# Kernel optimization log

Measured on AMD Instinct MI355X. Metric: run time of the kernel, lower is better.

The kernel has to match this reference:

```python
import jax, jax.numpy as jnp
import numpy as np

BUCKET_SIZE = 64
N_HASHES = 8
SELF_ATTN_VALUE = -5e4  # TOKEN_SELF_ATTN_VALUE
EPS = 1e-12  # F.normalize eps


def setup_inputs() -> dict:
    key = jax.random.key(0)
    k1, k2, k3 = jax.random.split(key, 3)
    B, S, D = 16, 4096, 128
    n_buckets = S // BUCKET_SIZE  # 64
    qk = jax.random.normal(k1, (B, S, D), dtype=jnp.float32)
    v = jax.random.normal(k2, (B, S, D), dtype=jnp.float32)
    # rotations_shape = (1, dim, n_hashes, n_buckets // 2); shared across batch
    rotations = jax.random.normal(k3, (1, D, N_HASHES, n_buckets // 2), dtype=jnp.float32)
    return {"qk": qk, "v": v, "rotations": rotations}


def _hash_vectors(qk, rotations, n_buckets):
    # qk: (B,S,D), rotations: (1,D,H,n_buckets//2)
    rotated = jnp.einsum('btf,fhi->bhti', qk, rotations[0])  # (B,H,S,nb/2)
    rotated = jnp.concatenate([rotated, -rotated], axis=-1)   # (B,H,S,nb)
    buckets = jnp.argmax(rotated, axis=-1)                    # (B,H,S)
    offsets = (jnp.arange(N_HASHES) * n_buckets)[None, :, None]
    return (buckets + offsets).reshape(qk.shape[0], -1)       # (B, H*S)


def _look_one_back(x):
    # concat each chunk with its predecessor (circular), along the window dim
    return jnp.concatenate([x, jnp.roll(x, 1, axis=1)], axis=2)


def reference(qk, v, rotations):
    B, S, D = qk.shape
    H = N_HASHES
    n_buckets = S // BUCKET_SIZE
    buckets = _hash_vectors(qk, rotations, n_buckets)         # (B, H*S) int

    ticker = jnp.broadcast_to(jnp.arange(H * S)[None, :], (B, H * S))
    buckets_and_t = S * buckets + (ticker % S)                # unique keys
    sticker = jnp.argsort(buckets_and_t, axis=-1)             # sort by bucket
    undo_sort = jnp.argsort(sticker, axis=-1)

    st = sticker % S                                          # original positions
    sqk = jnp.take_along_axis(qk, st[..., None], axis=1)      # (B,H*S,D)
    sv = jnp.take_along_axis(v, st[..., None], axis=1)

    C = H * n_buckets                                         # num chunks
    bq_t = st.reshape(B, C, -1)                               # (B,C,w)
    bqk = sqk.reshape(B, C, -1, D)
    bv = sv.reshape(B, C, -1, D)
    bq = bqk
    nrm = jnp.maximum(jnp.linalg.norm(bqk, axis=-1, keepdims=True), EPS)
    bk = bqk / nrm                                            # F.normalize

    bk = _look_one_back(bk)                                   # (B,C,2w,D)
    bv = _look_one_back(bv)
    bkv_t = _look_one_back(bq_t)                              # (B,C,2w)

    dots = jnp.einsum('bcie,bcje->bcij', bq, bk) * (D ** -0.5)  # (B,C,w,2w)
    self_mask = bq_t[:, :, :, None] == bkv_t[:, :, None, :]
    dots = jnp.where(self_mask, SELF_ATTN_VALUE, dots)

    lse = jax.scipy.special.logsumexp(dots, axis=-1, keepdims=True)
    probs = jnp.exp(dots - lse)
    bo = jnp.einsum('bcij,bcje->bcie', probs, bv)             # (B,C,w,D)

    so = bo.reshape(B, -1, D)                                 # (B,H*S,D)
    slogits = lse.reshape(B, -1)                              # (B,H*S)
    o = jnp.take_along_axis(so, undo_sort[..., None], axis=1)
    logits = jnp.take_along_axis(slogits, undo_sort, axis=1)

    o = o.reshape(B, H, S, D)
    logits = logits.reshape(B, H, S, 1)
    w = jnp.exp(logits - jax.scipy.special.logsumexp(logits, axis=1, keepdims=True))
    out = jnp.sum(o * w, axis=1)                              # (B,S,D)
    return out
```

## Files before the change

kernel.cpp:

```cpp
#include <hip/hip_runtime.h>
#include <hip/hip_bf16.h>


#define B_ 16
#define S_ 4096
#define D_ 128
#define H_ 8
#define C_ 512
#define SCALE_ 0.08838834764831845f

typedef __attribute__((ext_vector_type(8))) short bf16x8;
typedef __attribute__((ext_vector_type(8))) _Float16 f16x8;
typedef __attribute__((ext_vector_type(2))) _Float16 f16x2t;
typedef __attribute__((ext_vector_type(4))) float f32x4;
typedef __attribute__((ext_vector_type(2))) float f32x2v;
typedef __attribute__((ext_vector_type(4))) int int4v;

union BF8U { int4v i; bf16x8 b; };
union F16x8U { int4v i; f16x8 h; };

__device__ __forceinline__ unsigned hi_pack(float x0, float x1) {
    unsigned a, b;
    __builtin_memcpy(&b, &x0, 4);
    __builtin_memcpy(&a, &x1, 4);
    return __builtin_amdgcn_perm(a, b, 0x07060302u);
}
__device__ __forceinline__ float truncbf(float x) {
    unsigned u; __builtin_memcpy(&u, &x, 4);
    u &= 0xFFFF0000u;
    float f; __builtin_memcpy(&f, &u, 4);
    return f;
}
__device__ __forceinline__ unsigned pack2f16(float x0, float x1) {
    f16x2t h = {(_Float16)x0, (_Float16)x1};
    unsigned u; __builtin_memcpy(&u, &h, 4);
    return u;
}
__device__ __forceinline__ unsigned enc_ks(unsigned u) {
    return (u & 0x80000000u) ? ~u : (u | 0x80000000u);
}
__device__ __forceinline__ float dec_ks(unsigned ks) {
    unsigned u = (ks & 0x80000000u) ? (ks ^ 0x80000000u) : ~ks;
    float f; __builtin_memcpy(&f, &u, 4);
    return f;
}

__global__ __launch_bounds__(256) void norm_kernel(const float* __restrict__ qk,
                                                   float* __restrict__ rnrm) {
    int half = threadIdx.x >> 5;
    int lane32 = threadIdx.x & 31;
    size_t row = (size_t)blockIdx.x * 8 + half;
    float4 vv = ((const float4*)(qk + row * D_))[lane32];
    float ss = vv.x * vv.x + vv.y * vv.y + vv.z * vv.z + vv.w * vv.w;
    #pragma unroll
    for (int m = 1; m < 32; m <<= 1) ss += __shfl_xor(ss, m, 64);
    if (lane32 == 0) rnrm[row] = 1.0f / fmaxf(sqrtf(ss), 1e-12f);
}

__global__ __launch_bounds__(256) void prep_rot_kernel(const float* __restrict__ rot,
                                                       short* __restrict__ rth,
                                                       short* __restrict__ rtl) {
    int x = blockIdx.x * 256 + threadIdx.x;
    int hp = x >> 11;
    int ia = (x >> 5) & 63;
    int ft = x & 31;
    float v0 = rot[(size_t)(ft * 4 + 0) * 256 + hp * 64 + ia];
    float v1 = rot[(size_t)(ft * 4 + 1) * 256 + hp * 64 + ia];
    float v2 = rot[(size_t)(ft * 4 + 2) * 256 + hp * 64 + ia];
    float v3 = rot[(size_t)(ft * 4 + 3) * 256 + hp * 64 + ia];
    unsigned h0 = hi_pack(v0, v1), h1 = hi_pack(v2, v3);
    unsigned l0 = hi_pack(v0 - truncbf(v0), v1 - truncbf(v1));
    unsigned l1 = hi_pack(v2 - truncbf(v2), v3 - truncbf(v3));
    int off = ia * 128 + ((((ft >> 1) ^ (ia & 7)) << 3) | ((ft & 1) << 2));
    *(int2*)&rth[hp * 8192 + off] = make_int2((int)h0, (int)h1);
    *(int2*)&rtl[hp * 8192 + off] = make_int2((int)l0, (int)l1);
}

__global__ __launch_bounds__(256, 4) void hash_kernel(
        const float* __restrict__ qk, const float* __restrict__ rot,
        const short* __restrict__ rth, const short* __restrict__ rtl,
        int* __restrict__ buckets) {
    __shared__ unsigned char flags[2][64];

    const int bid = blockIdx.x;
    const int b = bid >> 8;
    const int tile = (bid >> 2) & 63;
    const int hp = bid & 3;
    const int tid = threadIdx.x;
    const int w = tid >> 6, l = tid & 63, g = l >> 4, m = l & 15;

    if (tid < 8) ((int4*)flags)[tid] = make_int4(0, 0, 0, 0);
    __syncthreads();

    const float* qrow = qk + ((size_t)b * S_ + (size_t)tile * 64 + w * 16 + m) * D_;
    bf16x8 qh[4], qlr[4];
    #pragma unroll
    for (int s = 0; s < 4; ++s) {
        float4 xa = *(const float4*)(qrow + s * 32 + g * 8);
        float4 xb = *(const float4*)(qrow + s * 32 + g * 8 + 4);
        BF8U hu, lu;
        hu.i[0] = (int)hi_pack(xa.x, xa.y); hu.i[1] = (int)hi_pack(xa.z, xa.w);
        hu.i[2] = (int)hi_pack(xb.x, xb.y); hu.i[3] = (int)hi_pack(xb.z, xb.w);
        lu.i[0] = (int)hi_pack(xa.x - truncbf(xa.x), xa.y - truncbf(xa.y));
        lu.i[1] = (int)hi_pack(xa.z - truncbf(xa.z), xa.w - truncbf(xa.w));
        lu.i[2] = (int)hi_pack(xb.x - truncbf(xb.x), xb.y - truncbf(xb.y));
        lu.i[3] = (int)hi_pack(xb.z - truncbf(xb.z), xb.w - truncbf(xb.w));
        qh[s] = hu.b; qlr[s] = lu.b;
    }

    f32x4 dots_n[4];
    #pragma unroll
    for (int nt = 0; nt < 4; ++nt) {
        f32x4 acc = (f32x4){0.f, 0.f, 0.f, 0.f};
        #pragma unroll
        for (int s = 0; s < 4; ++s) {
            int kr = hp * 8192 + (nt * 16 + m) * 128 + (((s * 4 + g) ^ (m & 7)) << 3);
            bf16x8 bh = *(const bf16x8*)&rth[kr];
            bf16x8 bl = *(const bf16x8*)&rtl[kr];
            acc = __builtin_amdgcn_mfma_f32_16x16x32_bf16(qh[s], bh, acc, 0, 0, 0);
            acc = __builtin_amdgcn_mfma_f32_16x16x32_bf16(qh[s], bl, acc, 0, 0, 0);
            acc = __builtin_amdgcn_mfma_f32_16x16x32_bf16(qlr[s], bh, acc, 0, 0, 0);
            acc = __builtin_amdgcn_mfma_f32_16x16x32_bf16(qlr[s], bl, acc, 0, 0, 0);
        }
        dots_n[nt] = acc;
    }

    #pragma unroll
    for (int hh = 0; hh < 2; ++hh) {
        int h = hp * 2 + hh;
        #pragma unroll
        for (int r = 0; r < 4; ++r) {
            unsigned long long kM = 0ull, kS = 0ull;
            #pragma unroll
            for (int nn = 0; nn < 2; ++nn) {
                float v = dots_n[hh * 2 + nn][r];
                unsigned u; __builtin_memcpy(&u, &v, 4);
                int i = nn * 16 + m;
                unsigned long long kp =
                    ((unsigned long long)enc_ks(u) << 6) | (unsigned)(63 - i);
                unsigned long long kn =
                    ((unsigned long long)enc_ks(u ^ 0x80000000u) << 6) |
                    (unsigned)(63 - (i + 32));
                if (kp > kM) { kS = kM; kM = kp; } else if (kp > kS) kS = kp;
                if (kn > kM) { kS = kM; kM = kn; } else if (kn > kS) kS = kn;
            }
            #pragma unroll
            for (int st = 1; st <= 8; st <<= 1) {
                unsigned long long oM = __shfl_xor(kM, st, 64);
                unsigned long long oS = __shfl_xor(kS, st, 64);
                unsigned long long lo = kM < oM ? kM : oM;
                kM = kM > oM ? kM : oM;
                unsigned long long hs = kS > oS ? kS : oS;
                kS = hs > lo ? hs : lo;
            }
            if (m == 0) {
                int tok = w * 16 + g * 4 + r;
                int i1 = 63 - (int)(kM & 63ull);
                float v1 = dec_ks((unsigned)(kM >> 6));
                float v2 = dec_ks((unsigned)(kS >> 6));
                if (v1 - v2 < 1e-3f) flags[hh][tok] = 1;
                buckets[(((size_t)(b * H_ + h)) << 12) + tile * 64 + tok] = i1;
            }
        }
    }
    __syncthreads();

    int tok = tid >> 2, part = tid & 3;
    const float* qtok = qk + ((size_t)b * S_ + (size_t)tile * 64 + tok) * D_;
    for (int hh = 0; hh < 2; ++hh) {
        if (!flags[hh][tok]) continue;
        int h = hp * 2 + hh;
        double pd[8] = {0, 0, 0, 0, 0, 0, 0, 0};
        #pragma unroll 2
        for (int f = 0; f < 128; ++f) {
            double q = (double)qtok[f];
            const float* rp = rot + (size_t)f * 256 + h * 32 + part * 8;
            float4 r0 = *(const float4*)rp;
            float4 r1 = *(const float4*)(rp + 4);
            pd[0] = fma(q, (double)r0.x, pd[0]);
            pd[1] = fma(q, (double)r0.y, pd[1]);
            pd[2] = fma(q, (double)r0.z, pd[2]);
            pd[3] = fma(q, (double)r0.w, pd[3]);
            pd[4] = fma(q, (double)r1.x, pd[4]);
            pd[5] = fma(q, (double)r1.y, pd[5]);
            pd[6] = fma(q, (double)r1.z, pd[6]);
            pd[7] = fma(q, (double)r1.w, pd[7]);
        }
        double bv = -1e300; int bi = 0;
        #pragma unroll
        for (int ii = 0; ii < 8; ++ii) {
            int i = part * 8 + ii;
            double v = pd[ii];
            if (v > bv || (v == bv && i < bi)) { bv = v; bi = i; }
            double nv = -v; int ni = i + 32;
            if (nv > bv || (nv == bv && ni < bi)) { bv = nv; bi = ni; }
        }
        #pragma unroll
        for (int mm = 1; mm <= 2; mm <<= 1) {
            double ov = __shfl_xor(bv, mm, 64);
            int oi = __shfl_xor(bi, mm, 64);
            if (ov > bv || (ov == bv && oi < bi)) { bv = ov; bi = oi; }
        }
        if (part == 0)
            buckets[(((size_t)(b * H_ + h)) << 12) + tile * 64 + tok] = bi;
    }
}

__global__ __launch_bounds__(256) void sort_kernel(const int* __restrict__ buckets,
                                                   int* __restrict__ st,
                                                   int* __restrict__ inv,
                                                   const float* __restrict__ rnrm,
                                                   float* __restrict__ rnrm_s) {
    __shared__ unsigned short hist[256][64];
    __shared__ int base[64];
    __shared__ int totals[64];
    int tid = threadIdx.x;
    const int* bkrow = buckets + (size_t)blockIdx.x * S_;
    const float* rnb = rnrm + (size_t)(blockIdx.x >> 3) * S_;

    unsigned int* h32 = (unsigned int*)hist;
    #pragma unroll
    for (int u = 0; u < 32; ++u) h32[u * 256 + tid] = 0;
    __syncthreads();

    #pragma unroll
    for (int u = 0; u < 16; ++u) {
        int t = tid * 16 + u;
        int bk = bkrow[t];
        hist[tid][bk]++;
    }
    __syncthreads();

    if (tid < 64) {
        int bucket = tid;
        int run = 0;
        for (int ch = 0; ch < 256; ++ch) {
            int v = hist[ch][bucket];
            hist[ch][bucket] = (unsigned short)run;
            run += v;
        }
        totals[bucket] = run;
    }
    __syncthreads();
    if (tid == 0) {
        int acc = 0;
        for (int k = 0; k < 64; ++k) { base[k] = acc; acc += totals[k]; }
    }
    __syncthreads();

    int* strow = st + (size_t)blockIdx.x * S_;
    int* invrow = inv + (size_t)blockIdx.x * S_;
    float* rnsrow = rnrm_s + (size_t)blockIdx.x * S_;
    #pragma unroll
    for (int u = 0; u < 16; ++u) {
        int t = tid * 16 + u;
        int bk = bkrow[t];
        int off = hist[tid][bk];
        hist[tid][bk] = (unsigned short)(off + 1);
        int pos = base[bk] + off;
        strow[pos] = t;
        invrow[t] = pos;
        rnsrow[pos] = rnb[t] * SCALE_;
    }
}

__device__ __forceinline__ void transpose4(const float4 v, int g, float (&w_)[4]) {
    bool b0 = (g & 1) != 0, b1 = (g & 2) != 0;
    float k0 = b1 ? v.z : v.x;
    float k1 = b1 ? v.w : v.y;
    float s0 = b1 ? v.x : v.z;
    float s1 = b1 ? v.y : v.w;
    float r0 = __shfl_xor(s0, 32, 64);
    float r1 = __shfl_xor(s1, 32, 64);
    float kq_ = b0 ? k1 : k0;
    float rq_ = b0 ? r1 : r0;
    float sk  = b0 ? k0 : k1;
    float sr  = b0 ? r0 : r1;
    float tk_ = __shfl_xor(sk, 16, 64);
    float tr_ = __shfl_xor(sr, 16, 64);
    float A0 = b0 ? tk_ : kq_;
    float A1 = b0 ? kq_ : tk_;
    float B0 = b0 ? tr_ : rq_;
    float B1 = b0 ? rq_ : tr_;
    w_[0] = b1 ? B0 : A0;
    w_[1] = b1 ? B1 : A1;
    w_[2] = b1 ? A0 : B0;
    w_[3] = b1 ? A1 : B1;
}

template<bool DENSE>
__global__ __launch_bounds__(256, 4) void attn_mfma_kernel(
        const float* __restrict__ qk, const float* __restrict__ rnrm_s,
        const float* __restrict__ vglob, const int* __restrict__ st,
        float* __restrict__ outnum, float* __restrict__ den,
        _Float16* __restrict__ snum, float* __restrict__ sden) {
    __shared__ int tq_s[64];
    __shared__ int tk1_s[64];
    __shared__ float rns0[64];
    __shared__ float rns1[64];
    __shared__ short kbuf[8192];
    __shared__ short vbuf[8192];

    const int p = blockIdx.x;
    const int bc = (p & 7) * 1024 + (p >> 3);
    const int b  = bc >> 9;
    const int c  = bc & 511;
    const int tid = threadIdx.x;
    const int w   = tid >> 6;
    const int l   = tid & 63;
    const int g   = l >> 4;
    const int m   = l & 15;
    const size_t bS = ((size_t)b << 12);
    const int* stb = st + ((size_t)b << 15);

    const int c1 = (c + 511) & 511;
    if (tid < 64) {
        tq_s[tid]  = stb[c * 64 + tid];
        tk1_s[tid] = stb[c1 * 64 + tid];
        rns0[tid] = rnrm_s[(((size_t)(b * H_ + (c >> 6))) << 12) + (size_t)(c & 63) * 64 + tid];
        rns1[tid] = rnrm_s[(((size_t)(b * H_ + (c1 >> 6))) << 12) + (size_t)(c1 & 63) * 64 + tid];
    }
    __syncthreads();

    const int qtok_m = tq_s[w * 16 + m];

    f16x8 qh[4];
    f32x4 e4[4];
    f32x4 acc_o[8];
    #pragma unroll
    for (int dt = 0; dt < 8; ++dt) acc_o[dt] = (f32x4){0.f, 0.f, 0.f, 0.f};
    float densum = 0.0f;

    float4 kreg[8];
    float4 va[4], vb[4];

    auto issue_k = [&](const int* __restrict__ toks) {
        #pragma unroll
        for (int u = 0; u < 8; ++u) {
            int token = u * 8 + (tid >> 5);
            int cc = tid & 31;
            kreg[u] = *(const float4*)(qk + (bS + toks[token]) * D_ + cc * 4);
        }
    };
    auto write_k = [&]() {
        #pragma unroll
        for (int u = 0; u < 8; ++u) {
            int token = u * 8 + (tid >> 5);
            int cc = tid & 31;
            float4 vv = kreg[u];
            unsigned h0 = pack2f16(vv.x, vv.y), h1 = pack2f16(vv.z, vv.w);
            int kw = token * 128 + ((((cc >> 1) ^ (token & 7)) << 3) | ((cc & 1) << 2));
            *(int2*)&kbuf[kw] = make_int2((int)h0, (int)h1);
        }
    };
    auto issue_v = [&](const int* __restrict__ toks) {
        #pragma unroll
        for (int up = 0; up < 4; ++up) {
            int kq8 = w * 16 + (up & 1) * 8;
            int cc = (up >> 1) * 16 + m;
            va[up] = *(const float4*)(vglob + (bS + toks[kq8 + g]) * D_ + cc * 4);
            vb[up] = *(const float4*)(vglob + (bS + toks[kq8 + 4 + g]) * D_ + cc * 4);
        }
    };
    auto write_v = [&]() {
        #pragma unroll
        for (int up = 0; up < 4; ++up) {
            int kq8 = w * 16 + (up & 1) * 8;
            int cc = (up >> 1) * 16 + m;
            float wa[4], wb[4];
            transpose4(va[up], g, wa);
            transpose4(vb[up], g, wb);
            unsigned h0 = pack2f16(wa[0], wa[1]), h1 = pack2f16(wa[2], wa[3]);
            unsigned h2 = pack2f16(wb[0], wb[1]), h3 = pack2f16(wb[2], wb[3]);
            int d = cc * 4 + g;
            int ds = d ^ ((d >> 3) & 7);
            int kg = kq8 >> 3;
            int idx = (kg * 128 + ds) * 8;
            *(int4*)&vbuf[idx] = make_int4((int)h0, (int)h1, (int)h2, (int)h3);
        }
    };
    auto qk_pass = [&](int mode, const float* __restrict__ rns,
                       const int* __restrict__ tkp) {
        #pragma unroll
        for (int kt = 0; kt < 4; ++kt) {
            f32x4 acc = (f32x4){0.f, 0.f, 0.f, 0.f};
            #pragma unroll
            for (int s4 = 0; s4 < 4; ++s4) {
                int kr = (kt * 16 + m) * 128 + (((s4 * 4 + g) ^ (m & 7)) << 3);
                f16x8 ah = *(const f16x8*)&kbuf[kr];
                acc = __builtin_amdgcn_mfma_f32_16x16x32_f16(ah, qh[s4], acc, 0, 0, 0);
            }
            f32x4 rn4 = *(const f32x4*)&rns[kt * 16 + g * 4];
            int4v kt4;
            if (mode == 1) kt4 = *(const int4v*)&tkp[kt * 16 + g * 4];
            f32x4 e;
            #pragma unroll
            for (int r = 0; r < 4; ++r) {
                float ev = __expf(acc[r] * rn4[r]);
                if (mode == 0) {
                    if (kt == w && (g * 4 + r) == m) ev = 0.0f;
                } else {
                    if (kt4[r] == qtok_m) ev = 0.0f;
                }
                e[r] = ev;
                densum += ev;
            }
            e4[kt] = e;
        }
    };
    auto pv_pass = [&]() {
        #pragma unroll
        for (int s = 0; s < 2; ++s) {
            float pav[8];
            #pragma unroll
            for (int c2 = 0; c2 < 2; ++c2) {
                int srcLane = ((g & 1) * 2 + c2) * 16 + m;
                #pragma unroll
                for (int r = 0; r < 4; ++r) {
                    float v0 = __shfl(e4[2 * s][r], srcLane, 64);
                    float v1 = __shfl(e4[2 * s + 1][r], srcLane, 64);
                    pav[c2 * 4 + r] = (g >> 1) ? v1 : v0;
                }
            }
            F16x8U pahu;
            #pragma unroll
            for (int j2 = 0; j2 < 4; ++j2)
                pahu.i[j2] = (int)pack2f16(pav[2 * j2], pav[2 * j2 + 1]);
            f16x8 pah = pahu.h;
            #pragma unroll
            for (int dt = 0; dt < 8; ++dt) {
                int d = dt * 16 + m;
                int ds = d ^ ((d >> 3) & 7);
                int base = ((s * 4 + g) * 128 + ds) * 8;
                f16x8 vh = *(const f16x8*)&vbuf[base];
                acc_o[dt] = __builtin_amdgcn_mfma_f32_16x16x32_f16(pah, vh, acc_o[dt], 0, 0, 0);
            }
        }
    };

    issue_k(tq_s);
    write_k();
    __syncthreads();

    #pragma unroll
    for (int s4 = 0; s4 < 4; ++s4) {
        int qr = (w * 16 + m) * 128 + (((s4 * 4 + g) ^ (m & 7)) << 3);
        qh[s4] = *(const f16x8*)&kbuf[qr];
    }
    issue_v(tq_s);
    qk_pass(0, rns0, tq_s);
    write_v();
    __syncthreads();

    issue_k(tk1_s);
    pv_pass();
    write_k();
    __syncthreads();

    issue_v(tk1_s);
    qk_pass(1, rns1, tk1_s);
    write_v();
    __syncthreads();

    pv_pass();

    densum += __shfl_xor(densum, 16, 64);
    densum += __shfl_xor(densum, 32, 64);

    if (DENSE) {
        const int h = c >> 6;
        const size_t base = (((size_t)(b * H_ + h)) << 12) + (size_t)(c & 63) * 64;
        #pragma unroll
        for (int r = 0; r < 4; ++r) {
            int row = w * 16 + g * 4 + r;
            _Float16* nrow = snum + (base + row) * D_;
            #pragma unroll
            for (int dt = 0; dt < 8; ++dt)
                __builtin_nontemporal_store((_Float16)acc_o[dt][r], nrow + dt * 16 + m);
        }
        if (g == 0) __builtin_nontemporal_store(densum, sden + base + w * 16 + m);
    } else {
        if (g == 0) atomicAdd(den + bS + qtok_m, densum);
        int4v q4tok = *(const int4v*)&tq_s[w * 16 + g * 4];
        #pragma unroll
        for (int r = 0; r < 4; ++r) {
            float* obase = outnum + ((bS + q4tok[r]) * D_);
            #pragma unroll
            for (int dt = 0; dt < 8; ++dt)
                atomicAdd(obase + dt * 16 + m, acc_o[dt][r]);
        }
    }
}

__global__ __launch_bounds__(256) void combine_kernel(
        const _Float16* __restrict__ snum, const float* __restrict__ sden,
        const int* __restrict__ inv, float* __restrict__ out) {
    int wv = threadIdx.x >> 6, l = threadIdx.x & 63;
    int t = blockIdx.x * 4 + wv;
    int b = t >> 12, s = t & 4095;
    float s0 = 0.f, s1 = 0.f, dsum = 0.f;
    #pragma unroll
    for (int h = 0; h < H_; ++h) {
        int bh = b * H_ + h;
        int pos = inv[((size_t)bh << 12) + s];
        size_t row = ((size_t)bh << 12) + pos;
        dsum += __builtin_nontemporal_load(sden + row);
        unsigned uv = __builtin_nontemporal_load(
            (const unsigned*)(snum + row * D_ + 2 * l));
        unsigned short us0 = (unsigned short)(uv & 0xFFFFu);
        unsigned short us1 = (unsigned short)(uv >> 16);
        _Float16 h0, h1;
        __builtin_memcpy(&h0, &us0, 2);
        __builtin_memcpy(&h1, &us1, 2);
        s0 += (float)h0;
        s1 += (float)h1;
    }
    float rd = 1.0f / dsum;
    f32x2v o2 = {s0 * rd, s1 * rd};
    __builtin_nontemporal_store(o2, (f32x2v*)(out + (size_t)t * D_ + 2 * l));
}

__global__ __launch_bounds__(256) void div_kernel(float* __restrict__ out,
                                                  const float* __restrict__ den) {
    int i = blockIdx.x * 256 + threadIdx.x;
    float4 o = ((float4*)out)[i];
    float dn = den[i >> 5];
    ((float4*)out)[i] = make_float4(o.x / dn, o.y / dn, o.z / dn, o.w / dn);
}

extern "C" void kernel_launch(void* const* d_in, const int* in_sizes, int n_in,
                              void* d_out, int out_size, void* d_ws, size_t ws_size,
                              hipStream_t stream) {
    const float* qk  = (const float*)d_in[0];
    const float* v   = (const float*)d_in[1];
    const float* rot = (const float*)d_in[2];
    float* out = (float*)d_out;

    char* ws = (char*)d_ws;
    float* rnrm    = (float*)ws;
    int* buckets   = (int*)(ws + 262144);
    int* inv       = buckets;
    int* st        = (int*)(ws + 2359296);
    float* rnrm_s  = (float*)(ws + 4456448);
    float* sden    = (float*)(ws + 6553600);
    short* rth     = (short*)(ws + 8650752);
    short* rtl     = (short*)(ws + 8716288);
    _Float16* snum = (_Float16*)(ws + 8781824);
    const size_t need = 8781824ull + 134217728ull;

    norm_kernel<<<B_ * S_ / 8, 256, 0, stream>>>(qk, rnrm);
    prep_rot_kernel<<<32, 256, 0, stream>>>(rot, rth, rtl);
    hash_kernel<<<B_ * (S_ / 64) * 4, 256, 0, stream>>>(qk, rot, rth, rtl, buckets);
    sort_kernel<<<B_ * H_, 256, 0, stream>>>(buckets, st, inv, rnrm, rnrm_s);

    if (ws_size >= need) {
        attn_mfma_kernel<true><<<B_ * C_, 256, 0, stream>>>(
            qk, rnrm_s, v, st, nullptr, nullptr, snum, sden);
        combine_kernel<<<B_ * S_ / 4, 256, 0, stream>>>(snum, sden, inv, out);
    } else {
        float* den = sden;
        hipMemsetAsync(out, 0, (size_t)B_ * S_ * D_ * 4, stream);
        hipMemsetAsync(den, 0, (size_t)B_ * S_ * 4, stream);
        attn_mfma_kernel<false><<<B_ * C_, 256, 0, stream>>>(
            qk, rnrm_s, v, st, out, den, nullptr, nullptr);
        div_kernel<<<B_ * S_ * D_ / 4 / 256, 256, 0, stream>>>(out, den);
    }
}
```

Measured before the change: 228.5 us.

## Process strips of consecutive chunks per block, reusing previous chunk's K/V tiles

```diff
diff --git a/kernel.cpp b/kernel.cpp
--- a/kernel.cpp
+++ b/kernel.cpp
@@ -7,6 +7,7 @@
 #define D_ 128
 #define H_ 8
 #define C_ 512
+#define L_ 8
 #define SCALE_ 0.08838834764831845f
 
 typedef __attribute__((ext_vector_type(8))) short bf16x8;
@@ -289,60 +290,42 @@
 }
 
 template<bool DENSE>
-__global__ __launch_bounds__(256, 4) void attn_mfma_kernel(
+__global__ __launch_bounds__(256, 2) void attn_strip_kernel(
         const float* __restrict__ qk, const float* __restrict__ rnrm_s,
         const float* __restrict__ vglob, const int* __restrict__ st,
         float* __restrict__ outnum, float* __restrict__ den,
         _Float16* __restrict__ snum, float* __restrict__ sden) {
-    __shared__ int tq_s[64];
-    __shared__ int tk1_s[64];
-    __shared__ float rns0[64];
-    __shared__ float rns1[64];
-    __shared__ short kbuf[8192];
-    __shared__ short vbuf[8192];
+    __shared__ int   toks[2][64];
+    __shared__ float rnss[2][64];
+    __shared__ short kbuf[2][8192];
+    __shared__ short vbuf[2][8192];
 
     const int p = blockIdx.x;
-    const int bc = (p & 7) * 1024 + (p >> 3);
-    const int b  = bc >> 9;
-    const int c  = bc & 511;
+    const int lg = (p & 7) * 128 + (p >> 3);
+    const int b = lg >> 6;
+    const int strip = lg & 63;
+    const int c0 = strip * L_;
     const int tid = threadIdx.x;
-    const int w   = tid >> 6;
-    const int l   = tid & 63;
-    const int g   = l >> 4;
-    const int m   = l & 15;
+    const int w = tid >> 6, l = tid & 63, g = l >> 4, m = l & 15;
     const size_t bS = ((size_t)b << 12);
     const int* stb = st + ((size_t)b << 15);
 
-    const int c1 = (c + 511) & 511;
-    if (tid < 64) {
-        tq_s[tid]  = stb[c * 64 + tid];
-        tk1_s[tid] = stb[c1 * 64 + tid];
-        rns0[tid] = rnrm_s[(((size_t)(b * H_ + (c >> 6))) << 12) + (size_t)(c & 63) * 64 + tid];
-        rns1[tid] = rnrm_s[(((size_t)(b * H_ + (c1 >> 6))) << 12) + (size_t)(c1 & 63) * 64 + tid];
-    }
-    __syncthreads();
-
-    const int qtok_m = tq_s[w * 16 + m];
-
-    f16x8 qh[4];
-    f32x4 e4[4];
-    f32x4 acc_o[8];
-    #pragma unroll
-    for (int dt = 0; dt < 8; ++dt) acc_o[dt] = (f32x4){0.f, 0.f, 0.f, 0.f};
-    float densum = 0.0f;
+    auto rns_base = [&](int c) -> size_t {
+        return (((size_t)(b * H_ + (c >> 6))) << 12) + (size_t)(c & 63) * 64;
+    };
 
     float4 kreg[8];
     float4 va[4], vb[4];
 
-    auto issue_k = [&](const int* __restrict__ toks) {
+    auto issue_k = [&](const int* __restrict__ tk) {
         #pragma unroll
         for (int u = 0; u < 8; ++u) {
             int token = u * 8 + (tid >> 5);
             int cc = tid & 31;
-            kreg[u] = *(const float4*)(qk + (bS + toks[token]) * D_ + cc * 4);
+            kreg[u] = *(const float4*)(qk + (bS + tk[token]) * D_ + cc * 4);
         }
     };
-    auto write_k = [&]() {
+    auto write_k = [&](short* __restrict__ kb) {
         #pragma unroll
         for (int u = 0; u < 8; ++u) {
             int token = u * 8 + (tid >> 5);
@@ -350,19 +333,19 @@
             float4 vv = kreg[u];
             unsigned h0 = pack2f16(vv.x, vv.y), h1 = pack2f16(vv.z, vv.w);
             int kw = token * 128 + ((((cc >> 1) ^ (token & 7)) << 3) | ((cc & 1) << 2));
-            *(int2*)&kbuf[kw] = make_int2((int)h0, (int)h1);
+            *(int2*)&kb[kw] = make_int2((int)h0, (int)h1);
         }
     };
-    auto issue_v = [&](const int* __restrict__ toks) {
+    auto issue_v = [&](const int* __restrict__ tk) {
         #pragma unroll
         for (int up = 0; up < 4; ++up) {
             int kq8 = w * 16 + (up & 1) * 8;
             int cc = (up >> 1) * 16 + m;
-            va[up] = *(const float4*)(vglob + (bS + toks[kq8 + g]) * D_ + cc * 4);
-            vb[up] = *(const float4*)(vglob + (bS + toks[kq8 + 4 + g]) * D_ + cc * 4);
+            va[up] = *(const float4*)(vglob + (bS + tk[kq8 + g]) * D_ + cc * 4);
+            vb[up] = *(const float4*)(vglob + (bS + tk[kq8 + 4 + g]) * D_ + cc * 4);
         }
     };
-    auto write_v = [&]() {
+    auto write_v = [&](short* __restrict__ vq) {
         #pragma unroll
         for (int up = 0; up < 4; ++up) {
             int kq8 = w * 16 + (up & 1) * 8;
@@ -376,118 +359,153 @@
             int ds = d ^ ((d >> 3) & 7);
             int kg = kq8 >> 3;
             int idx = (kg * 128 + ds) * 8;
-            *(int4*)&vbuf[idx] = make_int4((int)h0, (int)h1, (int)h2, (int)h3);
+            *(int4*)&vq[idx] = make_int4((int)h0, (int)h1, (int)h2, (int)h3);
         }
     };
-    auto qk_pass = [&](int mode, const float* __restrict__ rns,
-                       const int* __restrict__ tkp) {
-        #pragma unroll
-        for (int kt = 0; kt < 4; ++kt) {
-            f32x4 acc = (f32x4){0.f, 0.f, 0.f, 0.f};
+
+    const int cprev = (c0 + 511) & 511;
+    if (tid < 64) {
+        toks[1][tid] = stb[cprev * 64 + tid];
+        rnss[1][tid] = rnrm_s[rns_base(cprev) + tid];
+        toks[0][tid] = stb[c0 * 64 + tid];
+        rnss[0][tid] = rnrm_s[rns_base(c0) + tid];
+    }
+    __syncthreads();
+    issue_k(toks[1]);
+    issue_v(toks[1]);
+    write_k(kbuf[1]);
+    write_v(vbuf[1]);
+    __syncthreads();
+    issue_k(toks[0]);
+
+    #pragma unroll 1
+    for (int j = 0; j < L_; ++j) {
+        const int c = c0 + j;
+        const int cur = j & 1, prv = cur ^ 1;
+        short* kbc = kbuf[cur];
+        short* kbp = kbuf[prv];
+        short* vbc = vbuf[cur];
+        short* vbp = vbuf[prv];
+
+        write_k(kbc);
+        __syncthreads();
+
+        f16x8 qh[4];
+        #pragma unroll
+        for (int s4 = 0; s4 < 4; ++s4) {
+            int qr = (w * 16 + m) * 128 + (((s4 * 4 + g) ^ (m & 7)) << 3);
+            qh[s4] = *(const f16x8*)&kbc[qr];
+        }
+        const int qtok_m = toks[cur][w * 16 + m];
+        issue_v(toks[cur]);
+
+        f32x4 e4s[4], e4p[4];
+        float densum = 0.f;
+        auto qk_one = [&](const short* __restrict__ kb,
+                          const float* __restrict__ rns,
+                          const int* __restrict__ tkp, int mode,
+                          f32x4 (&e4)[4]) {
             #pragma unroll
-            for (int s4 = 0; s4 < 4; ++s4) {
-                int kr = (kt * 16 + m) * 128 + (((s4 * 4 + g) ^ (m & 7)) << 3);
-                f16x8 ah = *(const f16x8*)&kbuf[kr];
-                acc = __builtin_amdgcn_mfma_f32_16x16x32_f16(ah, qh[s4], acc, 0, 0, 0);
-            }
-            f32x4 rn4 = *(const f32x4*)&rns[kt * 16 + g * 4];
-            int4v kt4;
-            if (mode == 1) kt4 = *(const int4v*)&tkp[kt * 16 + g * 4];
-            f32x4 e;
+            for (int kt = 0; kt < 4; ++kt) {
+                f32x4 acc = (f32x4){0.f, 0.f, 0.f, 0.f};
+                #pragma unroll
+                for (int s4 = 0; s4 < 4; ++s4) {
+                    int kr = (kt * 16 + m) * 128 + (((s4 * 4 + g) ^ (m & 7)) << 3);
+                    f16x8 ah = *(const f16x8*)&kb[kr];
+                    acc = __builtin_amdgcn_mfma_f32_16x16x32_f16(ah, qh[s4], acc, 0, 0, 0);
+                }
+                f32x4 rn4 = *(const f32x4*)&rns[kt * 16 + g * 4];
+                int4v kt4;
+                if (mode == 1) kt4 = *(const int4v*)&tkp[kt * 16 + g * 4];
+                f32x4 e;
+                #pragma unroll
+                for (int r = 0; r < 4; ++r) {
+                    float ev = __expf(acc[r] * rn4[r]);
+                    if (mode == 0) {
+                        if (kt == w && (g * 4 + r) == m) ev = 0.0f;
+                    } else {
+                        if (kt4[r] == qtok_m) ev = 0.0f;
+                    }
+                    e[r] = ev;
+                    densum += ev;
+                }
+                e4[kt] = e;
+            }
+        };
+        qk_one(kbc, rnss[cur], toks[cur], 0, e4s);
+        qk_one(kbp, rnss[prv], toks[prv], 1, e4p);
+        __syncthreads();
+
+        if (j + 1 < L_ && tid < 64) {
+            int cn = c + 1;
+            toks[prv][tid] = stb[cn * 64 + tid];
+            rnss[prv][tid] = rnrm_s[rns_base(cn) + tid];
+        }
+        write_v(vbc);
+        __syncthreads();
+
+        if (j + 1 < L_) issue_k(toks[prv]);
+
+        f32x4 acc_o[8];
+        #pragma unroll
+        for (int dt = 0; dt < 8; ++dt) acc_o[dt] = (f32x4){0.f, 0.f, 0.f, 0.f};
+        auto pv_one = [&](const short* __restrict__ vq, const f32x4 (&e4)[4]) {
+            #pragma unroll
+            for (int s = 0; s < 2; ++s) {
+                float pav[8];
+                #pragma unroll
+                for (int c2 = 0; c2 < 2; ++c2) {
+                    int srcLane = ((g & 1) * 2 + c2) * 16 + m;
+                    #pragma unroll
+                    for (int r = 0; r < 4; ++r) {
+                        float v0 = __shfl(e4[2 * s][r], srcLane, 64);
+                        float v1 = __shfl(e4[2 * s + 1][r], srcLane, 64);
+                        pav[c2 * 4 + r] = (g >> 1) ? v1 : v0;
+                    }
+                }
+                F16x8U pahu;
+                #pragma unroll
+                for (int j2 = 0; j2 < 4; ++j2)
+                    pahu.i[j2] = (int)pack2f16(pav[2 * j2], pav[2 * j2 + 1]);
+                f16x8 pah = pahu.h;
+                #pragma unroll
+                for (int dt = 0; dt < 8; ++dt) {
+                    int d = dt * 16 + m;
+                    int ds = d ^ ((d >> 3) & 7);
+                    int base = ((s * 4 + g) * 128 + ds) * 8;
+                    f16x8 vh = *(const f16x8*)&vq[base];
+                    acc_o[dt] = __builtin_amdgcn_mfma_f32_16x16x32_f16(pah, vh, acc_o[dt], 0, 0, 0);
+                }
+            }
+        };
+        pv_one(vbc, e4s);
+        pv_one(vbp, e4p);
+
+        densum += __shfl_xor(densum, 16, 64);
+        densum += __shfl_xor(densum, 32, 64);
+
+        if (DENSE) {
+            const int h = c >> 6;
+            const size_t base = (((size_t)(b * H_ + h)) << 12) + (size_t)(c & 63) * 64;
             #pragma unroll
             for (int r = 0; r < 4; ++r) {
-                float ev = __expf(acc[r] * rn4[r]);
-                if (mode == 0) {
-                    if (kt == w && (g * 4 + r) == m) ev = 0.0f;
-                } else {
-                    if (kt4[r] == qtok_m) ev = 0.0f;
-                }
-                e[r] = ev;
-                densum += ev;
-            }
-            e4[kt] = e;
-        }
-    };
-    auto pv_pass = [&]() {
-        #pragma unroll
-        for (int s = 0; s < 2; ++s) {
-            float pav[8];
+                int row = w * 16 + g * 4 + r;
+                _Float16* nrow = snum + (base + row) * D_;
+                #pragma unroll
+                for (int dt = 0; dt < 8; ++dt)
+                    __builtin_nontemporal_store((_Float16)acc_o[dt][r], nrow + dt * 16 + m);
+            }
+            if (g == 0) __builtin_nontemporal_store(densum, sden + base + w * 16 + m);
+        } else {
+            if (g == 0) atomicAdd(den + bS + qtok_m, densum);
+            int4v q4tok = *(const int4v*)&toks[cur][w * 16 + g * 4];
             #pragma unroll
-            for (int c2 = 0; c2 < 2; ++c2) {
-                int srcLane = ((g & 1) * 2 + c2) * 16 + m;
-                #pragma unroll
-                for (int r = 0; r < 4; ++r) {
-                    float v0 = __shfl(e4[2 * s][r], srcLane, 64);
-                    float v1 = __shfl(e4[2 * s + 1][r], srcLane, 64);
-                    pav[c2 * 4 + r] = (g >> 1) ? v1 : v0;
-                }
-            }
-            F16x8U pahu;
-            #pragma unroll
-            for (int j2 = 0; j2 < 4; ++j2)
-                pahu.i[j2] = (int)pack2f16(pav[2 * j2], pav[2 * j2 + 1]);
-            f16x8 pah = pahu.h;
-            #pragma unroll
-            for (int dt = 0; dt < 8; ++dt) {
-                int d = dt * 16 + m;
-                int ds = d ^ ((d >> 3) & 7);
-                int base = ((s * 4 + g) * 128 + ds) * 8;
-                f16x8 vh = *(const f16x8*)&vbuf[base];
-                acc_o[dt] = __builtin_amdgcn_mfma_f32_16x16x32_f16(pah, vh, acc_o[dt], 0, 0, 0);
-            }
-        }
-    };
-
-    issue_k(tq_s);
-    write_k();
-    __syncthreads();
-
-    #pragma unroll
-    for (int s4 = 0; s4 < 4; ++s4) {
-        int qr = (w * 16 + m) * 128 + (((s4 * 4 + g) ^ (m & 7)) << 3);
-        qh[s4] = *(const f16x8*)&kbuf[qr];
-    }
-    issue_v(tq_s);
-    qk_pass(0, rns0, tq_s);
-    write_v();
-    __syncthreads();
-
-    issue_k(tk1_s);
-    pv_pass();
-    write_k();
-    __syncthreads();
-
-    issue_v(tk1_s);
-    qk_pass(1, rns1, tk1_s);
-    write_v();
-    __syncthreads();
-
-    pv_pass();
-
-    densum += __shfl_xor(densum, 16, 64);
-    densum += __shfl_xor(densum, 32, 64);
-
-    if (DENSE) {
-        const int h = c >> 6;
-        const size_t base = (((size_t)(b * H_ + h)) << 12) + (size_t)(c & 63) * 64;
-        #pragma unroll
-        for (int r = 0; r < 4; ++r) {
-            int row = w * 16 + g * 4 + r;
-            _Float16* nrow = snum + (base + row) * D_;
-            #pragma unroll
-            for (int dt = 0; dt < 8; ++dt)
-                __builtin_nontemporal_store((_Float16)acc_o[dt][r], nrow + dt * 16 + m);
-        }
-        if (g == 0) __builtin_nontemporal_store(densum, sden + base + w * 16 + m);
-    } else {
-        if (g == 0) atomicAdd(den + bS + qtok_m, densum);
-        int4v q4tok = *(const int4v*)&tq_s[w * 16 + g * 4];
-        #pragma unroll
-        for (int r = 0; r < 4; ++r) {
-            float* obase = outnum + ((bS + q4tok[r]) * D_);
-            #pragma unroll
-            for (int dt = 0; dt < 8; ++dt)
-                atomicAdd(obase + dt * 16 + m, acc_o[dt][r]);
+            for (int r = 0; r < 4; ++r) {
+                float* obase = outnum + ((bS + q4tok[r]) * D_);
+                #pragma unroll
+                for (int dt = 0; dt < 8; ++dt)
+                    atomicAdd(obase + dt * 16 + m, acc_o[dt][r]);
+            }
         }
     }
 }
@@ -554,14 +572,14 @@
     sort_kernel<<<B_ * H_, 256, 0, stream>>>(buckets, st, inv, rnrm, rnrm_s);
 
     if (ws_size >= need) {
-        attn_mfma_kernel<true><<<B_ * C_, 256, 0, stream>>>(
+        attn_strip_kernel<true><<<B_ * C_ / L_, 256, 0, stream>>>(
             qk, rnrm_s, v, st, nullptr, nullptr, snum, sden);
         combine_kernel<<<B_ * S_ / 4, 256, 0, stream>>>(snum, sden, inv, out);
     } else {
         float* den = sden;
         hipMemsetAsync(out, 0, (size_t)B_ * S_ * D_ * 4, stream);
         hipMemsetAsync(den, 0, (size_t)B_ * S_ * 4, stream);
-        attn_mfma_kernel<false><<<B_ * C_, 256, 0, stream>>>(
+        attn_strip_kernel<false><<<B_ * C_ / L_, 256, 0, stream>>>(
             qk, rnrm_s, v, st, out, den, nullptr, nullptr);
         div_kernel<<<B_ * S_ * D_ / 4 / 256, 256, 0, stream>>>(out, den);
     }
```

Measured after the change: 223.4 us, median of 2. 1.02x faster.
